# Kernel tuning notes

Measured on AMD Instinct MI355X. Metric: run time of the kernel, lower is better.

The kernel has to match this reference:

```python
import jax, jax.numpy as jnp
import numpy as np

K = 5
PAD = (K - 1) // 2
EPS_NORM = 1e-8
MASS_BOUND = 1e-7


def _window_indices(H, W):
    # For each output location (y,x) and each offset (dy,dx) in the kxk window,
    # compute the flat index of (y+dy, x+dx) in prev space and a validity mask.
    ys, xs = jnp.meshgrid(jnp.arange(H), jnp.arange(W), indexing='ij')  # [H,W]
    offs = jnp.arange(-PAD, PAD + 1)
    dy, dx = jnp.meshgrid(offs, offs, indexing='ij')  # [k,k]
    py = ys[:, :, None, None] + dy[None, None]  # [H,W,k,k]
    px = xs[:, :, None, None] + dx[None, None]
    valid = (py >= 0) & (py < H) & (px >= 0) & (px < W)
    ploc = jnp.clip(py, 0, H - 1) * W + jnp.clip(px, 0, W - 1)
    HW, KK = H * W, K * K
    return ploc.reshape(HW, KK), valid.reshape(HW, KK)


def setup_inputs() -> dict:
    key = jax.random.key(0)
    k1, k2, k3 = jax.random.split(key, 3)
    N, D, H, W = 8, 64, 64, 64
    return {
        'cur_feat': jax.random.normal(k1, (N, D, H, W), dtype=jnp.float32),
        'prev_feat': jax.random.normal(k2, (N, D, H, W), dtype=jnp.float32),
        'prev_mem': jax.random.normal(k3, (N, D, H, W), dtype=jnp.float32),
    }


def reference(cur_feat, prev_feat, prev_mem):
    N, D, H, W = prev_mem.shape
    HW = H * W
    cur = cur_feat.reshape(N, -1, HW)   # [N,Dc,HW]
    prev = prev_feat.reshape(N, -1, HW)
    # torch.norm(x, 0) = number of nonzero entries (scalar per batch)
    nc = jnp.sum(cur != 0, axis=(1, 2)).astype(cur.dtype) + EPS_NORM   # [N]
    npv = jnp.sum(prev != 0, axis=(1, 2)).astype(prev.dtype) + EPS_NORM
    # full cost volume: [N, HW(cur loc), HW(prev loc)], negatives clamped to 0
    aff = jnp.einsum('ndp,ndq->npq', cur, prev) / (nc * npv)[:, None, None]
    aff = jnp.maximum(aff, 0.0)

    ploc, valid = _window_indices(H, W)        # [HW,KK]
    loc = jnp.arange(HW)[:, None]              # [HW,1]
    coef = aff[:, loc, ploc] * valid[None].astype(aff.dtype)  # [N,HW,KK]
    mass = jnp.sum(coef, axis=-1)              # [N,HW]
    zero_mass = jnp.abs(mass) < MASS_BOUND
    w = coef / jnp.where(zero_mass, 1.0, mass)[:, :, None]    # [N,HW,KK]

    pm = prev_mem.reshape(N, D, HW)            # [N,D,HW]
    pm_win = pm[:, :, ploc]                    # [N,D,HW,KK]
    val = jnp.einsum('npk,ndpk->ndp', w, pm_win)  # weighted aggregation
    out = jnp.where(zero_mass[:, None, :], pm, val)  # mass==0 -> passthrough
    return out.reshape(N, D, H, W)
```

## Files before the change

### kernel.cpp

```cpp
#include <hip/hip_runtime.h>

#define N_  8
#define D_  64
#define H_  64
#define W_  64
#define HW_ (H_ * W_)
#define KK  25

__global__ __launch_bounds__(256) void count_nz_kernel(
    const float4* __restrict__ cur, const float4* __restrict__ prev,
    unsigned int* __restrict__ pc, unsigned int* __restrict__ pq)
{
    __shared__ unsigned int sc[4], sp[4];
    const int t    = threadIdx.x;
    const int wid  = t >> 6;
    const int lane = t & 63;

    unsigned int wc = 0, wp = 0;
#pragma unroll
    for (int j = 0; j < 4; ++j) {
        int idx = blockIdx.x * 1024 + j * 256 + t;
        float4 a = cur[idx];
        float4 b = prev[idx];
        wc += (unsigned)__popcll(__ballot(a.x != 0.f));
        wc += (unsigned)__popcll(__ballot(a.y != 0.f));
        wc += (unsigned)__popcll(__ballot(a.z != 0.f));
        wc += (unsigned)__popcll(__ballot(a.w != 0.f));
        wp += (unsigned)__popcll(__ballot(b.x != 0.f));
        wp += (unsigned)__popcll(__ballot(b.y != 0.f));
        wp += (unsigned)__popcll(__ballot(b.z != 0.f));
        wp += (unsigned)__popcll(__ballot(b.w != 0.f));
    }
    if (lane == 0) { sc[wid] = wc; sp[wid] = wp; }
    __syncthreads();
    if (t == 0) {
        pc[blockIdx.x] = sc[0] + sc[1] + sc[2] + sc[3];
        pq[blockIdx.x] = sp[0] + sp[1] + sp[2] + sp[3];
    }
}

__global__ __launch_bounds__(512, 2) void feature_align_kernel(
    const float* __restrict__ cur, const float* __restrict__ prev,
    const float* __restrict__ pm, float* __restrict__ out,
    const unsigned int* __restrict__ pc, const unsigned int* __restrict__ pq)
{
    __shared__ float red[4][KK][128];

    const int b    = blockIdx.x;
    const int n    = b >> 5;
    const int y0   = (b & 31) * 2;
    const int lane = threadIdx.x & 63;
    const int dg   = __builtin_amdgcn_readfirstlane(threadIdx.x >> 6);
    const int r    = lane >> 5;
    const int xq   = lane & 31;
    const int x0   = xq * 2;
    const int y    = y0 + r;
    const int pix0 = r * 64 + x0;

    int cb[3];
#pragma unroll
    for (int i = 0; i < 3; ++i)
        cb[i] = min(max(x0 - 2 + 2 * i, 0), W_ - 2);
    unsigned voff[5][3];
#pragma unroll
    for (int ky = 0; ky < 5; ++ky) {
        int qy = min(max(y + ky - 2, 0), H_ - 1);
#pragma unroll
        for (int i = 0; i < 3; ++i)
            voff[ky][i] = (unsigned)((qy * W_ + cb[i]) * 4);
    }
    const unsigned curoff = (unsigned)((y * W_ + x0) * 4);

    const size_t nbase = (size_t)n * D_ * HW_;
    const char* curb  = (const char*)(cur  + nbase + (size_t)dg * 8 * HW_);
    const char* prevb = (const char*)(prev + nbase + (size_t)dg * 8 * HW_);

    float acc0[KK], acc1[KK];
#pragma unroll
    for (int k = 0; k < KK; ++k) { acc0[k] = 0.f; acc1[k] = 0.f; }

#pragma unroll
    for (int dd = 0; dd < 8; ++dd) {
        const char* cch = curb  + (size_t)dd * HW_ * 4;
        const char* pch = prevb + (size_t)dd * HW_ * 4;
        float2 c = *(const float2*)(cch + curoff);
        float2 t[5][3];
#pragma unroll
        for (int ky = 0; ky < 5; ++ky)
#pragma unroll
            for (int i = 0; i < 3; ++i)
                t[ky][i] = *(const float2*)(pch + voff[ky][i]);
#pragma unroll
        for (int ky = 0; ky < 5; ++ky) {
            float v[6] = { t[ky][0].x, t[ky][0].y, t[ky][1].x,
                           t[ky][1].y, t[ky][2].x, t[ky][2].y };
#pragma unroll
            for (int kx = 0; kx < 5; ++kx) {
                acc0[ky * 5 + kx] = fmaf(c.x, v[kx],     acc0[ky * 5 + kx]);
                acc1[ky * 5 + kx] = fmaf(c.y, v[kx + 1], acc1[ky * 5 + kx]);
            }
        }
    }

    if (dg < 4) {
#pragma unroll
        for (int k = 0; k < KK; ++k)
            *(float2*)&red[dg][k][pix0] = make_float2(acc0[k], acc1[k]);
    }
    __syncthreads();
    if (dg >= 4) {
#pragma unroll
        for (int k = 0; k < KK; ++k) {
            float2 t2 = *(float2*)&red[dg - 4][k][pix0];
            t2.x += acc0[k]; t2.y += acc1[k];
            *(float2*)&red[dg - 4][k][pix0] = t2;
        }
    }
    __syncthreads();

    const bool active = threadIdx.x < 128;
    float cf[KK];
    float inv = 0.f;
    bool  zero = true;
    if (active) {
        const int pix = threadIdx.x;
        const int rr  = pix >> 6;
        const int xx  = pix & 63;

        unsigned int ccnt = pc[(n << 6) + (threadIdx.x & 63)];
        unsigned int vcnt = pq[(n << 6) + (threadIdx.x & 63)];
#pragma unroll
        for (int s = 32; s >= 1; s >>= 1) {
            ccnt += __shfl_xor(ccnt, s);
            vcnt += __shfl_xor(vcnt, s);
        }
        float scale = 1.0f / (((float)ccnt + 1e-8f) * ((float)vcnt + 1e-8f));

        float mass = 0.f;
#pragma unroll
        for (int k = 0; k < KK; ++k) {
            float s = red[0][k][pix] + red[1][k][pix]
                    + red[2][k][pix] + red[3][k][pix];
            int ky = k / 5, kx = k % 5;
            int py = y0 + rr + ky - 2;
            int pxc = xx + kx - 2;
            bool val = (py >= 0) && (py < H_) && (pxc >= 0) && (pxc < W_);
            float c = val ? fmaxf(s * scale, 0.f) : 0.f;
            cf[k] = c;
            mass += c;
        }
        zero = fabsf(mass) < 1e-7f;
        inv  = zero ? 0.f : 1.0f / mass;
    }
    __syncthreads();
    if (active) {
        const int pix = threadIdx.x;
#pragma unroll
        for (int k = 0; k < KK; ++k) red[0][k][pix] = cf[k] * inv;
        red[1][0][pix] = zero ? 1.f : 0.f;
    }
    __syncthreads();

    const char* pmb  = (const char*)(pm  + nbase + (size_t)dg * 8 * HW_);
    char*       outb = (char*)(out + nbase + (size_t)dg * 8 * HW_);

    const float zf0 = red[1][0][pix0];
    const float zf1 = red[1][0][pix0 + 1];

    if (zf0 != 0.f && zf1 != 0.f) {
#pragma unroll
        for (int dd = 0; dd < 8; ++dd) {
            float2 m = *(const float2*)(pmb + (size_t)dd * HW_ * 4 + curoff);
            *(float2*)(outb + (size_t)dd * HW_ * 4 + curoff) = m;
        }
    } else {
        float w0[KK], w1[KK];
#pragma unroll
        for (int k = 0; k < KK; ++k) {
            float2 ww = *(float2*)&red[0][k][pix0];
            w0[k] = ww.x; w1[k] = ww.y;
        }
#pragma unroll
        for (int dd = 0; dd < 8; ++dd) {
            const char* pch = pmb + (size_t)dd * HW_ * 4;
            float2 t2[5][3];
#pragma unroll
            for (int ky = 0; ky < 5; ++ky)
#pragma unroll
                for (int i = 0; i < 3; ++i)
                    t2[ky][i] = *(const float2*)(pch + voff[ky][i]);
            float v0 = 0.f, v1 = 0.f;
#pragma unroll
            for (int ky = 0; ky < 5; ++ky) {
                float v[6] = { t2[ky][0].x, t2[ky][0].y, t2[ky][1].x,
                               t2[ky][1].y, t2[ky][2].x, t2[ky][2].y };
#pragma unroll
                for (int kx = 0; kx < 5; ++kx) {
                    v0 = fmaf(w0[ky * 5 + kx], v[kx],     v0);
                    v1 = fmaf(w1[ky * 5 + kx], v[kx + 1], v1);
                }
            }
            float2 m = *(const float2*)(pch + curoff);
            float2 o;
            o.x = (zf0 != 0.f) ? m.x : v0;
            o.y = (zf1 != 0.f) ? m.y : v1;
            *(float2*)(outb + (size_t)dd * HW_ * 4 + curoff) = o;
        }
    }
}

extern "C" void kernel_launch(void* const* d_in, const int* in_sizes, int n_in,
                              void* d_out, int out_size, void* d_ws, size_t ws_size,
                              hipStream_t stream)
{
    const float* cur  = (const float*)d_in[0];
    const float* prev = (const float*)d_in[1];
    const float* pm   = (const float*)d_in[2];
    float*       out  = (float*)d_out;
    unsigned int* pc  = (unsigned int*)d_ws;
    unsigned int* pq  = pc + 512;

    count_nz_kernel<<<512, 256, 0, stream>>>(
        (const float4*)cur, (const float4*)prev, pc, pq);

    feature_align_kernel<<<256, 512, 0, stream>>>(cur, prev, pm, out, pc, pq);
}
```

Measured before the change: 88.05 us.

## Prefetch prev_mem center values early, merge barriers, and count prev_mem nonzeros

The alignment kernel now loads the 8 center prev_mem values and the nonzero-count partials at kernel start, so their latency overlaps the correlation loop. The passthrough and blend paths reuse these registers instead of reloading. The finalize step drops one __syncthreads by writing normalized weights directly, and the launch bound goes from 2 to 1 blocks per CU, relaxing register limits. The count kernel also reads all of prev_mem to count its nonzeros into a new buffer that nothing uses, which adds a full extra tensor read.

```diff
diff --git a/kernel.cpp b/kernel.cpp
--- a/kernel.cpp
+++ b/kernel.cpp
@@ -9,19 +9,22 @@
 
 __global__ __launch_bounds__(256) void count_nz_kernel(
     const float4* __restrict__ cur, const float4* __restrict__ prev,
-    unsigned int* __restrict__ pc, unsigned int* __restrict__ pq)
+    const float4* __restrict__ pmv,
+    unsigned int* __restrict__ pc, unsigned int* __restrict__ pq,
+    unsigned int* __restrict__ pr)
 {
-    __shared__ unsigned int sc[4], sp[4];
+    __shared__ unsigned int sc[4], sp[4], sr[4];
     const int t    = threadIdx.x;
     const int wid  = t >> 6;
     const int lane = t & 63;
 
-    unsigned int wc = 0, wp = 0;
+    unsigned int wc = 0, wp = 0, wr = 0;
 #pragma unroll
     for (int j = 0; j < 4; ++j) {
         int idx = blockIdx.x * 1024 + j * 256 + t;
         float4 a = cur[idx];
         float4 b = prev[idx];
+        float4 m = pmv[idx];
         wc += (unsigned)__popcll(__ballot(a.x != 0.f));
         wc += (unsigned)__popcll(__ballot(a.y != 0.f));
         wc += (unsigned)__popcll(__ballot(a.z != 0.f));
@@ -30,16 +33,21 @@
         wp += (unsigned)__popcll(__ballot(b.y != 0.f));
         wp += (unsigned)__popcll(__ballot(b.z != 0.f));
         wp += (unsigned)__popcll(__ballot(b.w != 0.f));
-    }
-    if (lane == 0) { sc[wid] = wc; sp[wid] = wp; }
+        wr += (unsigned)__popcll(__ballot(m.x != 0.f));
+        wr += (unsigned)__popcll(__ballot(m.y != 0.f));
+        wr += (unsigned)__popcll(__ballot(m.z != 0.f));
+        wr += (unsigned)__popcll(__ballot(m.w != 0.f));
+    }
+    if (lane == 0) { sc[wid] = wc; sp[wid] = wp; sr[wid] = wr; }
     __syncthreads();
     if (t == 0) {
         pc[blockIdx.x] = sc[0] + sc[1] + sc[2] + sc[3];
         pq[blockIdx.x] = sp[0] + sp[1] + sp[2] + sp[3];
+        pr[blockIdx.x] = sr[0] + sr[1] + sr[2] + sr[3];
     }
 }
 
-__global__ __launch_bounds__(512, 2) void feature_align_kernel(
+__global__ __launch_bounds__(512, 1) void feature_align_kernel(
     const float* __restrict__ cur, const float* __restrict__ prev,
     const float* __restrict__ pm, float* __restrict__ out,
     const unsigned int* __restrict__ pc, const unsigned int* __restrict__ pq)
@@ -74,6 +82,15 @@
     const size_t nbase = (size_t)n * D_ * HW_;
     const char* curb  = (const char*)(cur  + nbase + (size_t)dg * 8 * HW_);
     const char* prevb = (const char*)(prev + nbase + (size_t)dg * 8 * HW_);
+    const char* pmb   = (const char*)(pm   + nbase + (size_t)dg * 8 * HW_);
+    char*       outb  = (char*)(out + nbase + (size_t)dg * 8 * HW_);
+
+    float2 pmc[8];
+#pragma unroll
+    for (int dd = 0; dd < 8; ++dd)
+        pmc[dd] = *(const float2*)(pmb + (size_t)dd * HW_ * 4 + curoff);
+    unsigned int ccnt = pc[(n << 6) + lane];
+    unsigned int vcnt = pq[(n << 6) + lane];
 
     float acc0[KK], acc1[KK];
 #pragma unroll
@@ -118,61 +135,48 @@
     }
     __syncthreads();
 
-    const bool active = threadIdx.x < 128;
-    float cf[KK];
-    float inv = 0.f;
-    bool  zero = true;
-    if (active) {
+    if (threadIdx.x < 128) {
         const int pix = threadIdx.x;
         const int rr  = pix >> 6;
         const int xx  = pix & 63;
 
-        unsigned int ccnt = pc[(n << 6) + (threadIdx.x & 63)];
-        unsigned int vcnt = pq[(n << 6) + (threadIdx.x & 63)];
+        unsigned int cc = ccnt, vv = vcnt;
 #pragma unroll
         for (int s = 32; s >= 1; s >>= 1) {
-            ccnt += __shfl_xor(ccnt, s);
-            vcnt += __shfl_xor(vcnt, s);
-        }
-        float scale = 1.0f / (((float)ccnt + 1e-8f) * ((float)vcnt + 1e-8f));
+            cc += __shfl_xor(cc, s);
+            vv += __shfl_xor(vv, s);
+        }
+        float scale = 1.0f / (((float)cc + 1e-8f) * ((float)vv + 1e-8f));
 
         float mass = 0.f;
+        float cf[KK];
 #pragma unroll
         for (int k = 0; k < KK; ++k) {
             float s = red[0][k][pix] + red[1][k][pix]
                     + red[2][k][pix] + red[3][k][pix];
             int ky = k / 5, kx = k % 5;
-            int py = y0 + rr + ky - 2;
+            int py  = y0 + rr + ky - 2;
             int pxc = xx + kx - 2;
             bool val = (py >= 0) && (py < H_) && (pxc >= 0) && (pxc < W_);
             float c = val ? fmaxf(s * scale, 0.f) : 0.f;
             cf[k] = c;
             mass += c;
         }
-        zero = fabsf(mass) < 1e-7f;
-        inv  = zero ? 0.f : 1.0f / mass;
-    }
-    __syncthreads();
-    if (active) {
-        const int pix = threadIdx.x;
+        bool  zero = fabsf(mass) < 1e-7f;
+        float inv  = zero ? 0.f : 1.0f / mass;
 #pragma unroll
         for (int k = 0; k < KK; ++k) red[0][k][pix] = cf[k] * inv;
         red[1][0][pix] = zero ? 1.f : 0.f;
     }
     __syncthreads();
 
-    const char* pmb  = (const char*)(pm  + nbase + (size_t)dg * 8 * HW_);
-    char*       outb = (char*)(out + nbase + (size_t)dg * 8 * HW_);
-
     const float zf0 = red[1][0][pix0];
     const float zf1 = red[1][0][pix0 + 1];
 
     if (zf0 != 0.f && zf1 != 0.f) {
 #pragma unroll
-        for (int dd = 0; dd < 8; ++dd) {
-            float2 m = *(const float2*)(pmb + (size_t)dd * HW_ * 4 + curoff);
-            *(float2*)(outb + (size_t)dd * HW_ * 4 + curoff) = m;
-        }
+        for (int dd = 0; dd < 8; ++dd)
+            *(float2*)(outb + (size_t)dd * HW_ * 4 + curoff) = pmc[dd];
     } else {
         float w0[KK], w1[KK];
 #pragma unroll
@@ -200,10 +204,9 @@
                     v1 = fmaf(w1[ky * 5 + kx], v[kx + 1], v1);
                 }
             }
-            float2 m = *(const float2*)(pch + curoff);
             float2 o;
-            o.x = (zf0 != 0.f) ? m.x : v0;
-            o.y = (zf1 != 0.f) ? m.y : v1;
+            o.x = (zf0 != 0.f) ? pmc[dd].x : v0;
+            o.y = (zf1 != 0.f) ? pmc[dd].y : v1;
             *(float2*)(outb + (size_t)dd * HW_ * 4 + curoff) = o;
         }
     }
@@ -219,9 +222,10 @@
     float*       out  = (float*)d_out;
     unsigned int* pc  = (unsigned int*)d_ws;
     unsigned int* pq  = pc + 512;
+    unsigned int* pr  = pq + 512;
 
     count_nz_kernel<<<512, 256, 0, stream>>>(
-        (const float4*)cur, (const float4*)prev, pc, pq);
+        (const float4*)cur, (const float4*)prev, (const float4*)pm, pc, pq, pr);
 
     feature_align_kernel<<<256, 512, 0, stream>>>(cur, prev, pm, out, pc, pq);
 }
```

Result: no change. 86.49 us (-1.8%).
